# Optimization experiments

Hardware: AMD Instinct MI355X
Metric: run time of the kernel (lower is better)

The kernel has to match this reference:

```python
import jax, jax.numpy as jnp
import numpy as np
import math

B, N, E, H, DEPTH, MLP_RATIO, A = 8, 1024, 768, 12, 6, 4, 7
F = MLP_RATIO * E


def _get_attention_slopes(n):
    def p2(n):
        start = 2 ** (-2 ** (-(math.log2(n) - 3)))
        return [start * start ** i for i in range(n)]
    if math.log2(n).is_integer():
        return p2(n)
    c = 2 ** math.floor(math.log2(n))
    return p2(c) + _get_attention_slopes(2 * c)[0::2][: n - c]


def _ln(x, scale, bias, eps=1e-6):
    m = jnp.mean(x, axis=-1, keepdims=True)
    v = jnp.var(x, axis=-1, keepdims=True)
    return (x - m) * jax.lax.rsqrt(v + eps) * scale + bias


def setup_inputs() -> dict:
    key = jax.random.key(0)
    ks = jax.random.split(key, 8)
    s = 0.02
    return {
        "x": jax.random.normal(ks[0], (B, N, E), jnp.float32),
        "ln1_scale": jnp.ones((DEPTH, E), jnp.float32),
        "ln1_bias": jnp.zeros((DEPTH, E), jnp.float32),
        "wqkv": jax.random.normal(ks[1], (DEPTH, E, 3 * E), jnp.float32) * s,
        "bqkv": jnp.zeros((DEPTH, 3 * E), jnp.float32),
        "wo": jax.random.normal(ks[2], (DEPTH, E, E), jnp.float32) * s,
        "bo": jnp.zeros((DEPTH, E), jnp.float32),
        "ln2_scale": jnp.ones((DEPTH, E), jnp.float32),
        "ln2_bias": jnp.zeros((DEPTH, E), jnp.float32),
        "w1": jax.random.normal(ks[3], (DEPTH, E, F), jnp.float32) * s,
        "w2": jax.random.normal(ks[4], (DEPTH, F, E), jnp.float32) * s,
        "lnf_scale": jnp.ones((E,), jnp.float32),
        "lnf_bias": jnp.zeros((E,), jnp.float32),
        "head_w1": jax.random.normal(ks[5], (E, E), jnp.float32) * s,
        "head_b1": jnp.zeros((E,), jnp.float32),
        "head_w2": jax.random.normal(ks[6], (E, A), jnp.float32) * s,
    }


def reference(x, ln1_scale, ln1_bias, wqkv, bqkv, wo, bo, ln2_scale, ln2_bias, w1, w2, lnf_scale, lnf_bias, head_w1, head_b1, head_w2):
    b, n, e = x.shape
    h = H
    dh = e // h
    scale = dh ** (-0.5)
    # ALiBi bias: slopes[h] * key-position (exactly as original code computes it)
    slopes = jnp.asarray(_get_attention_slopes(h), x.dtype)
    pos_bias = slopes[None, :, None, None] * jnp.arange(n, dtype=x.dtype)[None, None, None, :]
    causal = jnp.tril(jnp.ones((n, n), bool))[None, None]  # [1,1,n,n]
    big_neg = jnp.finfo(x.dtype).min

    depth = ln1_scale.shape[0]
    for i in range(depth):
        y = _ln(x, ln1_scale[i], ln1_bias[i])
        qkv = y @ wqkv[i] + bqkv[i]
        q, k, v = jnp.split(qkv, 3, axis=-1)
        q = q.reshape(b, n, h, dh).transpose(0, 2, 1, 3)  # b h n d
        k = k.reshape(b, n, h, dh).transpose(0, 2, 1, 3)
        v = v.reshape(b, n, h, dh).transpose(0, 2, 1, 3)
        att = jnp.einsum('bhnd,bhmd->bhnm', q, k) * scale + pos_bias
        att = jnp.where(causal, att, big_neg)
        att = jax.nn.softmax(att, axis=-1)
        o = jnp.einsum('bhnm,bhmd->bhnd', att, v)
        o = o.transpose(0, 2, 1, 3).reshape(b, n, e)
        x = x + (o @ wo[i] + bo[i])
        y = _ln(x, ln2_scale[i], ln2_bias[i])
        y = jax.nn.gelu(y @ w1[i])  # flax default: tanh-approx gelu; FF has no bias
        x = x + y @ w2[i]
    x = _ln(x, lnf_scale, lnf_bias)
    actions = jax.nn.relu(x @ head_w1 + head_b1) @ head_w2
    return actions
```

## Files before the change

### kernel.cpp

```cpp
#include <hip/hip_runtime.h>
#include <hip/hip_bf16.h>
#include <cstdint>

#define DEV __device__ __forceinline__

typedef __bf16 bf16x8 __attribute__((ext_vector_type(8)));
typedef float f32x4 __attribute__((ext_vector_type(4)));
typedef unsigned short u16;
typedef u16 u16x8 __attribute__((ext_vector_type(8)));
typedef u16 u16x4 __attribute__((ext_vector_type(4)));
typedef uint32_t u32x2 __attribute__((ext_vector_type(2)));

DEV u16 f2bf(float f) {
  union { float f; uint32_t u; } a; a.f = f;
  uint32_t u = a.u + 0x7fffu + ((a.u >> 16) & 1u);
  return (u16)(u >> 16);
}
DEV float b2f(u16 v) {
  union { uint32_t u; float f; } a; a.u = ((uint32_t)v) << 16;
  return a.f;
}

DEV float fexp2(float x) {
#if __has_builtin(__builtin_amdgcn_exp2f)
  return __builtin_amdgcn_exp2f(x);
#else
  return __expf(x * 0.69314718056f);
#endif
}

DEV uint32_t cvtpk(float lo, float hi) {
  uint32_t r;
  asm("v_cvt_pk_bf16_f32 %0, %1, %2" : "=v"(r) : "v"(lo), "v"(hi));
  return r;
}

DEV void gload16(const void* g, void* lds) {
  __builtin_amdgcn_global_load_lds((__attribute__((address_space(1))) void*)g,
                                   (__attribute__((address_space(3))) void*)lds,
                                   16, 0, 0);
}

struct TMat { const float* src; u16* dst; int K; int N; int t0; };
struct TArgs { TMat m[26]; int nmat; };

__global__ __launch_bounds__(256) void transpose_all(TArgs args) {
  __shared__ float tile[64][65];
  const int bid = blockIdx.x;
  int i = 0;
  #pragma unroll 1
  for (int t = 1; t < args.nmat; ++t) if (bid >= args.m[t].t0) i = t;
  const TMat mm = args.m[i];
  const int tid = bid - mm.t0;
  const int ntx = mm.N >> 6;
  const int tx = tid % ntx, ty = tid / ntx;
  const int n0 = tx * 64, k0 = ty * 64;
  const int c = threadIdx.x & 63, r0 = threadIdx.x >> 6;
  #pragma unroll
  for (int s = 0; s < 16; ++s) {
    int r = r0 + s * 4;
    tile[r][c] = mm.src[(size_t)(k0 + r) * mm.N + n0 + c];
  }
  __syncthreads();
  #pragma unroll
  for (int s = 0; s < 16; ++s) {
    int rr = r0 + s * 4;
    mm.dst[(size_t)(n0 + rr) * mm.K + k0 + c] = f2bf(tile[c][rr]);
  }
}

__global__ __launch_bounds__(256) void ln_kernel(const float* __restrict__ x,
                                                 const float* __restrict__ sc,
                                                 const float* __restrict__ bi,
                                                 u16* __restrict__ y, int Mtok) {
  const int tok = (blockIdx.x * blockDim.x + threadIdx.x) >> 6;
  const int l = threadIdx.x & 63;
  if (tok >= Mtok) return;
  const float4* row = (const float4*)(x + (size_t)tok * 768);
  float4 a = row[l], b = row[l + 64], cc = row[l + 128];
  float s = a.x + a.y + a.z + a.w + b.x + b.y + b.z + b.w + cc.x + cc.y + cc.z + cc.w;
  float q = a.x*a.x + a.y*a.y + a.z*a.z + a.w*a.w
          + b.x*b.x + b.y*b.y + b.z*b.z + b.w*b.w
          + cc.x*cc.x + cc.y*cc.y + cc.z*cc.z + cc.w*cc.w;
  #pragma unroll
  for (int off = 1; off < 64; off <<= 1) { s += __shfl_xor(s, off); q += __shfl_xor(q, off); }
  const float mean = s * (1.f / 768.f);
  const float var = q * (1.f / 768.f) - mean * mean;
  const float r = rsqrtf(var + 1e-6f);
  u16* yr = y + (size_t)tok * 768;
  #pragma unroll
  for (int p = 0; p < 3; ++p) {
    const int col0 = 4 * (l + 64 * p);
    float4 v = (p == 0) ? a : (p == 1) ? b : cc;
    float4 scv = *(const float4*)(sc + col0);
    float4 biv = *(const float4*)(bi + col0);
    u16x4 o;
    o[0] = f2bf((v.x - mean) * r * scv.x + biv.x);
    o[1] = f2bf((v.y - mean) * r * scv.y + biv.y);
    o[2] = f2bf((v.z - mean) * r * scv.z + biv.z);
    o[3] = f2bf((v.w - mean) * r * scv.w + biv.w);
    *(u16x4*)(yr + col0) = o;
  }
}

enum { EPI_BF16 = 0, EPI_RESID = 1, EPI_GELU = 2, EPI_RELU = 3 };

__global__ __launch_bounds__(256, 2) void gemm128(
    const u16* __restrict__ A, const u16* __restrict__ Bt,
    const float* __restrict__ bias, const float* __restrict__ resid,
    float* __restrict__ outF, u16* __restrict__ outB,
    int N, int K, int nxb, int epi) {
  __shared__ u16 smem[32768];
  const int tid = threadIdx.x;
  const int w = tid >> 6, l = tid & 63;

  const int nwg = gridDim.x;
  const int flat = blockIdx.x;
  const int wg = (flat & 7) * (nwg >> 3) + (flat >> 3);
  const int bx = wg % nxb, by = wg / nxb;
  const int m0 = by << 7, n0 = bx << 7;

  const int wr = (w >> 1) << 6, wc = (w & 1) << 6;
  const int cl = l & 15, g = l >> 4;
  f32x4 acc[4][4] = {};

  const int lrow = l >> 3;
  const int scol = ((l & 7) ^ lrow) << 3;
  const u16* agp = A  + (size_t)(m0 + (w << 5) + lrow) * K + scol;
  const u16* bgp = Bt + (size_t)(n0 + (w << 5) + lrow) * K + scol;
  const int ldso = w << 11;
  const int nkt = K >> 6;

  #pragma unroll
  for (int q = 0; q < 4; ++q) {
    gload16(agp + (size_t)(q * 8) * K, &smem[ldso + (q << 9)]);
    gload16(bgp + (size_t)(q * 8) * K, &smem[16384 + ldso + (q << 9)]);
  }
  __syncthreads();

  const int sw = cl & 7;
  for (int kt = 0; kt < nkt; ++kt) {
    const int cur = kt & 1;
    if (kt + 1 < nkt) {
      const size_t koff = (size_t)(kt + 1) << 6;
      const int nb = (cur ^ 1) << 13;
      #pragma unroll
      for (int q = 0; q < 4; ++q) {
        gload16(agp + koff + (size_t)(q * 8) * K, &smem[nb + ldso + (q << 9)]);
        gload16(bgp + koff + (size_t)(q * 8) * K, &smem[16384 + nb + ldso + (q << 9)]);
      }
    }
    const u16* Ab = &smem[cur << 13];
    const u16* Bb = &smem[16384 + (cur << 13)];
    #pragma unroll
    for (int ks = 0; ks < 2; ++ks) {
      bf16x8 af[4], bfr[4];
      const int ps = (((ks << 2) | g) ^ sw) << 3;
      #pragma unroll
      for (int mt = 0; mt < 4; ++mt)
        af[mt] = *(const bf16x8*)(Ab + ((wr + mt * 16 + cl) << 6) + ps);
      #pragma unroll
      for (int nt = 0; nt < 4; ++nt)
        bfr[nt] = *(const bf16x8*)(Bb + ((wc + nt * 16 + cl) << 6) + ps);
      #pragma unroll
      for (int mt = 0; mt < 4; ++mt)
        #pragma unroll
        for (int nt = 0; nt < 4; ++nt)
          acc[mt][nt] = __builtin_amdgcn_mfma_f32_16x16x32_bf16(af[mt], bfr[nt], acc[mt][nt], 0, 0, 0);
    }
    __syncthreads();
  }

  float* scr = (float*)smem + w * 1056;
  const int rg = g << 2;
  const int er = l >> 3;
  const int ec0 = (l & 7) << 3;
  #pragma unroll
  for (int mt = 0; mt < 4; ++mt) {
    #pragma unroll
    for (int nt = 0; nt < 4; ++nt)
      #pragma unroll
      for (int j = 0; j < 4; ++j)
        scr[(rg + j) * 66 + nt * 16 + cl] = acc[mt][nt][j];
    #pragma unroll
    for (int t = 0; t < 2; ++t) {
      const int r = (t << 3) + er;
      const int grow = m0 + wr + mt * 16 + r;
      const int gcol = n0 + wc + ec0;
      float v[8];
      #pragma unroll
      for (int u = 0; u < 8; ++u) v[u] = scr[r * 66 + ec0 + u];
      if (bias) {
        #pragma unroll
        for (int u = 0; u < 8; ++u) v[u] += bias[gcol + u];
      }
      if (epi == EPI_RESID) {
        const float* rp = resid + (size_t)grow * N + gcol;
        float* op = outF + (size_t)grow * N + gcol;
        float4 o0, o1;
        o0.x = v[0] + rp[0]; o0.y = v[1] + rp[1]; o0.z = v[2] + rp[2]; o0.w = v[3] + rp[3];
        o1.x = v[4] + rp[4]; o1.y = v[5] + rp[5]; o1.z = v[6] + rp[6]; o1.w = v[7] + rp[7];
        *(float4*)op = o0;
        *(float4*)(op + 4) = o1;
      } else {
        u16x8 ov;
        #pragma unroll
        for (int u = 0; u < 8; ++u) {
          float x = v[u];
          if (epi == EPI_GELU) {
            const float e = __expf(-(1.5957691216f * x + 0.0713548163f * x * x * x));
            x = x / (1.f + e);
          } else if (epi == EPI_RELU) {
            x = fmaxf(x, 0.f);
          }
          ov[u] = f2bf(x);
        }
        *(u16x8*)(outB + (size_t)grow * N + gcol) = ov;
      }
    }
  }
}

__global__ __launch_bounds__(512, 2) void attn_kernel(const u16* __restrict__ qkv,
                                                      u16* __restrict__ o) {
  __shared__ u16 Ksm[2][4096];
  __shared__ u16 Vt[2][64][68];
  __shared__ u16 P[8][16][72];
  const int flat = blockIdx.x;
  const int b = flat & 7;
  const int rr = flat >> 3;
  const int h = rr >> 3;
  const int j = rr & 7;
  const int tid = threadIdx.x;
  const int w = tid >> 6, l = tid & 63;
  const int cl = l & 15, lg = l >> 4;
  const int qtile = (w < 4) ? j : 15 - j;
  const int q0 = qtile * 64 + (w & 3) * 16;
  const int rowg = q0 + cl;
  const float log2e = 1.44269504f;
  const float scale2 = 0.125f * log2e;
  const float slope = (h < 8) ? exp2f(-(float)(h + 1)) : exp2f(-0.5f - (float)(h - 8));
  const float slope2 = slope * log2e;
  const size_t rs_ = 2304;
  const size_t bbase = (size_t)b * 1024 * rs_;

  const u16* qp = qkv + bbase + (size_t)rowg * rs_ + h * 64 + lg * 8;
  bf16x8 qa0 = *(const bf16x8*)qp;
  bf16x8 qa1 = *(const bf16x8*)(qp + 32);

  float m_r = -1e30f, l_r = 0.f;
  f32x4 oacc[4];
  #pragma unroll
  for (int d = 0; d < 4; ++d) oacc[d] = (f32x4){0.f, 0.f, 0.f, 0.f};

  const u16* ksrc = qkv + bbase + (size_t)(tid >> 3) * rs_ + 768 + h * 64 +
                    (((tid & 7) ^ ((tid >> 3) & 7)) << 3);
  const int vd0 = w << 3;
  const u16* vbase = qkv + bbase + (size_t)l * rs_ + 1536 + h * 64 + vd0;

  const int nkv = 16 - j;
  gload16(ksrc, &Ksm[0][w << 9]);
  u16x8 vreg = *(const u16x8*)vbase;
  __syncthreads();

  const int sw = cl & 7;
  const int ps0 = (lg ^ sw) << 3;
  const int ps1 = ps0 ^ 32;

  for (int kv = 0; kv < nkv; ++kv) {
    const int buf = kv & 1;
    #pragma unroll
    for (int i = 0; i < 8; ++i) Vt[buf][vd0 + i][l] = vreg[i];
    u16x8 vnext = vreg;
    if (kv + 1 < nkv) {
      gload16(ksrc + (size_t)(kv + 1) * 64 * rs_, &Ksm[buf ^ 1][w << 9]);
      vnext = *(const u16x8*)(vbase + (size_t)(kv + 1) * 64 * rs_);
    }

    const bool active = (kv <= qtile);
    bf16x8 pa0, pa1;
    if (active) {
      const u16* Kb = &Ksm[buf][0];
      f32x4 pp[4];
      float pm = -3.0e38f;
      __builtin_amdgcn_s_setprio(1);
      #pragma unroll
      for (int nt = 0; nt < 4; ++nt) {
        const int row = nt * 16 + cl;
        bf16x8 bk0 = *(const bf16x8*)(Kb + (row << 6) + ps0);
        bf16x8 bk1 = *(const bf16x8*)(Kb + (row << 6) + ps1);
        f32x4 s = (f32x4){0.f, 0.f, 0.f, 0.f};
        s = __builtin_amdgcn_mfma_f32_16x16x32_bf16(bk0, qa0, s, 0, 0, 0);
        s = __builtin_amdgcn_mfma_f32_16x16x32_bf16(bk1, qa1, s, 0, 0, 0);
        const int kb = kv * 64 + nt * 16 + (lg << 2);
        #pragma unroll
        for (int jj = 0; jj < 4; ++jj) {
          const int colg = kb + jj;
          float v = s[jj] * scale2 + slope2 * (float)colg;
          pp[nt][jj] = (colg <= rowg) ? v : -3.0e38f;
        }
        pm = fmaxf(pm, fmaxf(fmaxf(pp[nt][0], pp[nt][1]),
                             fmaxf(pp[nt][2], pp[nt][3])));
      }
      __builtin_amdgcn_s_setprio(0);
      pm = fmaxf(pm, __shfl_xor(pm, 16));
      pm = fmaxf(pm, __shfl_xor(pm, 32));
      const float mnew = fmaxf(m_r, pm);
      const float al = fexp2(m_r - mnew);
      m_r = mnew;
      float rs = 0.f;
      #pragma unroll
      for (int nt = 0; nt < 4; ++nt) {
        #pragma unroll
        for (int jj = 0; jj < 4; ++jj) {
          float p = fexp2(pp[nt][jj] - m_r);
          pp[nt][jj] = p;
          rs += p;
        }
      }
      rs += __shfl_xor(rs, 16);
      rs += __shfl_xor(rs, 32);
      l_r = l_r * al + rs;
      float a4[4];
      #pragma unroll
      for (int jj = 0; jj < 4; ++jj) a4[jj] = __shfl(al, (lg << 2) + jj);
      #pragma unroll
      for (int d = 0; d < 4; ++d)
        #pragma unroll
        for (int jj = 0; jj < 4; ++jj) oacc[d][jj] *= a4[jj];
      #pragma unroll
      for (int nt = 0; nt < 4; ++nt) {
        u32x2 pr;
        pr[0] = cvtpk(pp[nt][0], pp[nt][1]);
        pr[1] = cvtpk(pp[nt][2], pp[nt][3]);
        *(u32x2*)&P[w][cl][nt * 16 + (lg << 2)] = pr;
      }
      pa0 = *(const bf16x8*)&P[w][cl][lg * 8];
      pa1 = *(const bf16x8*)&P[w][cl][32 + lg * 8];
    }

    __syncthreads();

    if (active) {
      __builtin_amdgcn_s_setprio(1);
      #pragma unroll
      for (int d = 0; d < 4; ++d) {
        bf16x8 bv0 = *(const bf16x8*)&Vt[buf][d * 16 + cl][lg * 8];
        bf16x8 bv1 = *(const bf16x8*)&Vt[buf][d * 16 + cl][32 + lg * 8];
        oacc[d] = __builtin_amdgcn_mfma_f32_16x16x32_bf16(pa0, bv0, oacc[d], 0, 0, 0);
        oacc[d] = __builtin_amdgcn_mfma_f32_16x16x32_bf16(pa1, bv1, oacc[d], 0, 0, 0);
      }
      __builtin_amdgcn_s_setprio(0);
    }
    vreg = vnext;
  }

  const float linv = 1.f / l_r;
  float i4[4];
  #pragma unroll
  for (int jj = 0; jj < 4; ++jj) i4[jj] = __shfl(linv, (lg << 2) + jj);
  u16* op = o + ((size_t)b * 1024 + q0) * 768 + h * 64;
  #pragma unroll
  for (int d = 0; d < 4; ++d)
    #pragma unroll
    for (int jj = 0; jj < 4; ++jj)
      op[(size_t)((lg << 2) + jj) * 768 + d * 16 + cl] = f2bf(oacc[d][jj] * i4[jj]);
}

__global__ __launch_bounds__(256) void head2_kernel(const u16* __restrict__ act,
                                                    const float* __restrict__ w,
                                                    float* __restrict__ out, int Mtok) {
  const int tok = (blockIdx.x * blockDim.x + threadIdx.x) >> 6;
  const int l = threadIdx.x & 63;
  if (tok >= Mtok) return;
  float s[7] = {0.f, 0.f, 0.f, 0.f, 0.f, 0.f, 0.f};
  const u16* ar = act + (size_t)tok * 768;
  #pragma unroll
  for (int i = 0; i < 12; ++i) {
    const int k = l + i * 64;
    const float a = b2f(ar[k]);
    #pragma unroll
    for (int j = 0; j < 7; ++j) s[j] += a * w[k * 7 + j];
  }
  #pragma unroll
  for (int off = 32; off; off >>= 1)
    #pragma unroll
    for (int j = 0; j < 7; ++j) s[j] += __shfl_down(s[j], off);
  if (l == 0) {
    #pragma unroll
    for (int j = 0; j < 7; ++j) out[(size_t)tok * 7 + j] = s[j];
  }
}

extern "C" void kernel_launch(void* const* d_in, const int* in_sizes, int n_in,
                              void* d_out, int out_size, void* d_ws, size_t ws_size,
                              hipStream_t stream) {
  const float* x_in = (const float*)d_in[0];
  const float* ln1s = (const float*)d_in[1];
  const float* ln1b = (const float*)d_in[2];
  const float* wqkv = (const float*)d_in[3];
  const float* bqkv = (const float*)d_in[4];
  const float* wo   = (const float*)d_in[5];
  const float* bo   = (const float*)d_in[6];
  const float* ln2s = (const float*)d_in[7];
  const float* ln2b = (const float*)d_in[8];
  const float* w1   = (const float*)d_in[9];
  const float* w2   = (const float*)d_in[10];
  const float* lnfs = (const float*)d_in[11];
  const float* lnfb = (const float*)d_in[12];
  const float* hw1  = (const float*)d_in[13];
  const float* hb1  = (const float*)d_in[14];
  const float* hw2  = (const float*)d_in[15];
  float* out = (float*)d_out;

  const int Mtok = 8192, E = 768, E3 = 2304, F = 3072, DEPTH = 6;

  char* ws = (char*)d_ws;
  size_t off = 0;
  auto alloc = [&](size_t bytes) -> char* {
    char* p = ws + off; off += (bytes + 255) & ~(size_t)255; return p;
  };
  u16*  wqkvt = (u16*)alloc((size_t)DEPTH * E3 * E * 2);
  u16*  wot   = (u16*)alloc((size_t)DEPTH * E * E * 2);
  u16*  w1t   = (u16*)alloc((size_t)DEPTH * F * E * 2);
  u16*  w2t   = (u16*)alloc((size_t)DEPTH * E * F * 2);
  u16*  hw1t  = (u16*)alloc((size_t)E * E * 2);
  float* xb   = (float*)alloc((size_t)Mtok * E * 4);
  u16*  yb    = (u16*)alloc((size_t)Mtok * E * 2);
  u16*  big   = (u16*)alloc((size_t)Mtok * F * 2);
  (void)ws_size; (void)in_sizes; (void)n_in; (void)out_size;

  TArgs ta; int nm = 0; int t0 = 0;
  auto add = [&](const float* s, u16* d, int K, int N) {
    ta.m[nm].src = s; ta.m[nm].dst = d; ta.m[nm].K = K; ta.m[nm].N = N; ta.m[nm].t0 = t0;
    t0 += (N / 64) * (K / 64); ++nm;
  };
  for (int i = 0; i < DEPTH; ++i) add(wqkv + (size_t)i * E * E3, wqkvt + (size_t)i * E3 * E, E, E3);
  for (int i = 0; i < DEPTH; ++i) add(wo + (size_t)i * E * E, wot + (size_t)i * E * E, E, E);
  for (int i = 0; i < DEPTH; ++i) add(w1 + (size_t)i * E * F, w1t + (size_t)i * F * E, E, F);
  for (int i = 0; i < DEPTH; ++i) add(w2 + (size_t)i * F * E, w2t + (size_t)i * E * F, F, E);
  add(hw1, hw1t, E, E);
  ta.nmat = nm;
  transpose_all<<<t0, 256, 0, stream>>>(ta);

  u16* qkvb = big;
  for (int i = 0; i < DEPTH; ++i) {
    const float* xsrc = (i == 0) ? x_in : xb;
    ln_kernel<<<Mtok / 4, 256, 0, stream>>>(xsrc, ln1s + i * E, ln1b + i * E, yb, Mtok);
    gemm128<<<18 * 64, 256, 0, stream>>>(yb, wqkvt + (size_t)i * E3 * E, bqkv + (size_t)i * E3,
                                         nullptr, nullptr, qkvb, E3, E, 18, EPI_BF16);
    attn_kernel<<<768, 512, 0, stream>>>(qkvb, yb);
    gemm128<<<6 * 64, 256, 0, stream>>>(yb, wot + (size_t)i * E * E, bo + (size_t)i * E,
                                        xsrc, xb, nullptr, E, E, 6, EPI_RESID);
    ln_kernel<<<Mtok / 4, 256, 0, stream>>>(xb, ln2s + i * E, ln2b + i * E, yb, Mtok);
    gemm128<<<24 * 64, 256, 0, stream>>>(yb, w1t + (size_t)i * F * E, nullptr,
                                         nullptr, nullptr, big, F, E, 24, EPI_GELU);
    gemm128<<<6 * 64, 256, 0, stream>>>(big, w2t + (size_t)i * E * F, nullptr,
                                        xb, xb, nullptr, E, F, 6, EPI_RESID);
  }
  ln_kernel<<<Mtok / 4, 256, 0, stream>>>(xb, lnfs, lnfb, yb, Mtok);
  gemm128<<<6 * 64, 256, 0, stream>>>(yb, hw1t, hb1, nullptr, nullptr, big,
                                      E, E, 6, EPI_RELU);
  head2_kernel<<<Mtok / 4, 256, 0, stream>>>(big, hw2, out, Mtok);
}
```

Measured before the change: 1.501 ms.

## Halve GEMM K-tile to raise occupancy, add nontemporal stores and token remap

The GEMM K-tile shrinks from 64 to 32, which halves shared memory (16K u16) so launch bounds can ask for 4 workgroups per CU instead of 2. The LDS swizzle and load layout are reworked to match. BF16 and GELU GEMM outputs now use nontemporal stores. The layernorm and head2 kernels remap block index to token with an XCD-style interleave. More K iterations mean more barriers per tile and less latency hiding per stage. Nontemporal stores on outputs that the next kernel reads could cost cache hits.

```diff
diff --git a/kernel.cpp b/kernel.cpp
--- a/kernel.cpp
+++ b/kernel.cpp
@@ -39,6 +39,10 @@
   __builtin_amdgcn_global_load_lds((__attribute__((address_space(1))) void*)g,
                                    (__attribute__((address_space(3))) void*)lds,
                                    16, 0, 0);
+}
+
+DEV void nts8(u16* p, u16x8 v) {
+  __builtin_nontemporal_store(v, (u16x8*)p);
 }
 
 struct TMat { const float* src; u16* dst; int K; int N; int t0; };
@@ -73,7 +77,8 @@
                                                  const float* __restrict__ sc,
                                                  const float* __restrict__ bi,
                                                  u16* __restrict__ y, int Mtok) {
-  const int tok = (blockIdx.x * blockDim.x + threadIdx.x) >> 6;
+  const int bid = blockIdx.x;
+  const int tok = ((bid & 7) << 10) + ((bid >> 3) << 2) + (threadIdx.x >> 6);
   const int l = threadIdx.x & 63;
   if (tok >= Mtok) return;
   const float4* row = (const float4*)(x + (size_t)tok * 768);
@@ -105,12 +110,12 @@
 
 enum { EPI_BF16 = 0, EPI_RESID = 1, EPI_GELU = 2, EPI_RELU = 3 };
 
-__global__ __launch_bounds__(256, 2) void gemm128(
+__global__ __launch_bounds__(256, 4) void gemm128(
     const u16* __restrict__ A, const u16* __restrict__ Bt,
     const float* __restrict__ bias, const float* __restrict__ resid,
     float* __restrict__ outF, u16* __restrict__ outB,
     int N, int K, int nxb, int epi) {
-  __shared__ u16 smem[32768];
+  __shared__ u16 smem[16384];
   const int tid = threadIdx.x;
   const int w = tid >> 6, l = tid & 63;
 
@@ -124,50 +129,44 @@
   const int cl = l & 15, g = l >> 4;
   f32x4 acc[4][4] = {};
 
-  const int lrow = l >> 3;
-  const int scol = ((l & 7) ^ lrow) << 3;
-  const u16* agp = A  + (size_t)(m0 + (w << 5) + lrow) * K + scol;
-  const u16* bgp = Bt + (size_t)(n0 + (w << 5) + lrow) * K + scol;
-  const int ldso = w << 11;
-  const int nkt = K >> 6;
-
-  #pragma unroll
-  for (int q = 0; q < 4; ++q) {
-    gload16(agp + (size_t)(q * 8) * K, &smem[ldso + (q << 9)]);
-    gload16(bgp + (size_t)(q * 8) * K, &smem[16384 + ldso + (q << 9)]);
-  }
+  const int srow = (w << 4) + (l >> 2);
+  const int scol = (((l & 3) ^ ((l >> 2) & 3) ^ ((l >> 4) & 3)) << 3);
+  const u16* agp = A  + (size_t)(m0 + srow) * K + scol;
+  const u16* bgp = Bt + (size_t)(n0 + srow) * K + scol;
+  const int dst = w << 9;
+  const int nkt = K >> 5;
+
+  gload16(agp,                     &smem[dst]);
+  gload16(agp + (size_t)64 * K,    &smem[2048 + dst]);
+  gload16(bgp,                     &smem[8192 + dst]);
+  gload16(bgp + (size_t)64 * K,    &smem[8192 + 2048 + dst]);
   __syncthreads();
 
-  const int sw = cl & 7;
+  const int ps = ((g ^ (cl & 3) ^ ((cl >> 2) & 3)) << 3);
   for (int kt = 0; kt < nkt; ++kt) {
     const int cur = kt & 1;
     if (kt + 1 < nkt) {
-      const size_t koff = (size_t)(kt + 1) << 6;
-      const int nb = (cur ^ 1) << 13;
-      #pragma unroll
-      for (int q = 0; q < 4; ++q) {
-        gload16(agp + koff + (size_t)(q * 8) * K, &smem[nb + ldso + (q << 9)]);
-        gload16(bgp + koff + (size_t)(q * 8) * K, &smem[16384 + nb + ldso + (q << 9)]);
-      }
+      const int ko = (kt + 1) << 5;
+      const int nb = (cur ^ 1) << 12;
+      gload16(agp + ko,                  &smem[nb + dst]);
+      gload16(agp + ko + (size_t)64 * K, &smem[nb + 2048 + dst]);
+      gload16(bgp + ko,                  &smem[8192 + nb + dst]);
+      gload16(bgp + ko + (size_t)64 * K, &smem[8192 + nb + 2048 + dst]);
     }
-    const u16* Ab = &smem[cur << 13];
-    const u16* Bb = &smem[16384 + (cur << 13)];
-    #pragma unroll
-    for (int ks = 0; ks < 2; ++ks) {
-      bf16x8 af[4], bfr[4];
-      const int ps = (((ks << 2) | g) ^ sw) << 3;
-      #pragma unroll
-      for (int mt = 0; mt < 4; ++mt)
-        af[mt] = *(const bf16x8*)(Ab + ((wr + mt * 16 + cl) << 6) + ps);
+    const u16* Ab = &smem[cur << 12];
+    const u16* Bb = &smem[8192 + (cur << 12)];
+    bf16x8 af[4], bfr[4];
+    #pragma unroll
+    for (int mt = 0; mt < 4; ++mt)
+      af[mt] = *(const bf16x8*)(Ab + ((wr + mt * 16 + cl) << 5) + ps);
+    #pragma unroll
+    for (int nt = 0; nt < 4; ++nt)
+      bfr[nt] = *(const bf16x8*)(Bb + ((wc + nt * 16 + cl) << 5) + ps);
+    #pragma unroll
+    for (int mt = 0; mt < 4; ++mt)
       #pragma unroll
       for (int nt = 0; nt < 4; ++nt)
-        bfr[nt] = *(const bf16x8*)(Bb + ((wc + nt * 16 + cl) << 6) + ps);
-      #pragma unroll
-      for (int mt = 0; mt < 4; ++mt)
-        #pragma unroll
-        for (int nt = 0; nt < 4; ++nt)
-          acc[mt][nt] = __builtin_amdgcn_mfma_f32_16x16x32_bf16(af[mt], bfr[nt], acc[mt][nt], 0, 0, 0);
-    }
+        acc[mt][nt] = __builtin_amdgcn_mfma_f32_16x16x32_bf16(af[mt], bfr[nt], acc[mt][nt], 0, 0, 0);
     __syncthreads();
   }
 
@@ -215,7 +214,10 @@
           }
           ov[u] = f2bf(x);
         }
-        *(u16x8*)(outB + (size_t)grow * N + gcol) = ov;
+        if (epi == EPI_BF16 || epi == EPI_GELU)
+          nts8(outB + (size_t)grow * N + gcol, ov);
+        else
+          *(u16x8*)(outB + (size_t)grow * N + gcol) = ov;
       }
     }
   }
@@ -370,7 +372,8 @@
 __global__ __launch_bounds__(256) void head2_kernel(const u16* __restrict__ act,
                                                     const float* __restrict__ w,
                                                     float* __restrict__ out, int Mtok) {
-  const int tok = (blockIdx.x * blockDim.x + threadIdx.x) >> 6;
+  const int bid = blockIdx.x;
+  const int tok = ((bid & 7) << 10) + ((bid >> 3) << 2) + (threadIdx.x >> 6);
   const int l = threadIdx.x & 63;
   if (tok >= Mtok) return;
   float s[7] = {0.f, 0.f, 0.f, 0.f, 0.f, 0.f, 0.f};
```

After: 1.577 ms. +5.1%, slower.
